# Kernel tuning notes

Measured on AMD Instinct MI355X. Metric: run time of the kernel, lower is better.

The kernel has to match this reference:

```python
import jax, jax.numpy as jnp
import numpy as np

D, N, P, K = 128, 500000, 1024, 32


def setup_inputs() -> dict:
    key = jax.random.key(0)
    k1, k2, k3, k4 = jax.random.split(key, 4)
    U_base = jax.random.normal(k1, (D, N), dtype=jnp.float32)
    U = jax.random.normal(k2, (D, P), dtype=jnp.float32)
    # ragged partition: column j of U_base belongs to group seg_ids[j]
    merge_idx = jnp.arange(N, dtype=jnp.int64)
    seg_ids = jnp.sort(jax.random.randint(k3, (N,), 0, P)).astype(jnp.int64)
    # k nearest-neighbor indices per group for the Gram gather
    G = jax.random.randint(k4, (P, K), 0, P).astype(jnp.int64)
    return {"U_base": U_base, "U": U, "merge_idx": merge_idx,
            "seg_ids": seg_ids, "G": G}


def reference(U_base, U, merge_idx, seg_ids, G):
    # Flattened ragged loop: for each column j in group g = seg_ids[j],
    # dot(U[:, g], U_base[:, merge_idx[j]]); sum over dim 0 then square.
    dots = jnp.sum(U_base[:, merge_idx] * U[:, seg_ids], axis=0)  # [N]
    loss = -0.5 * jnp.sum(dots ** 2)
    # Gram-matrix neighbor gather: (U.T @ U)[G] -> [P, K, P]
    gram = U.T @ U  # [P, P]
    loss = loss - 0.5 * jnp.mean(gram[G] ** 2)
    return loss
```

## Files before the change

kernel.cpp:

```cpp
#include <hip/hip_runtime.h>

#define DIM 128
#define NCOLS 500000
#define PP 1024
#define KK 32


__global__ void init_ws_kernel(float* __restrict__ wsf) {
    int i = blockIdx.x * blockDim.x + threadIdx.x;
    if (i < 2) wsf[i] = 0.0f;
    int* counts = (int*)(wsf + 2);
    if (i < PP) counts[i] = 0;
}

__global__ void hist_kernel(const int* __restrict__ G, int* __restrict__ counts) {
    int i = blockIdx.x * blockDim.x + threadIdx.x;
    if (i < PP * KK) atomicAdd(&counts[G[i]], 1);
}

__global__ void gram_m_kernel(const float* __restrict__ U, float* __restrict__ M) {
    int t = blockIdx.x * blockDim.x + threadIdx.x;
    int d = t >> 7, e = t & 127;
    const float4* ud = (const float4*)(U + (size_t)d * PP);
    const float4* ue = (const float4*)(U + (size_t)e * PP);
    float acc = 0.0f;
#pragma unroll 4
    for (int p = 0; p < PP / 4; ++p) {
        float4 a = ud[p], b = ue[p];
        acc += a.x * b.x + a.y * b.y + a.z * b.z + a.w * b.w;
    }
    M[t] = acc;
}

__global__ void rowsq_kernel(const float* __restrict__ U, const float* __restrict__ M,
                             const int* __restrict__ counts, float* __restrict__ acc_out) {
    __shared__ float u_s[DIM];
    __shared__ float red[DIM];
    int r = blockIdx.x;
    int d = threadIdx.x;
    u_s[d] = U[(size_t)d * PP + r];
    __syncthreads();
    float t = 0.0f;
#pragma unroll 8
    for (int e = 0; e < DIM; ++e)
        t += M[e * DIM + d] * u_s[e];
    float v = u_s[d] * t;
    red[d] = v;
    __syncthreads();
    for (int s = 64; s > 0; s >>= 1) {
        if (d < s) red[d] += red[d + s];
        __syncthreads();
    }
    if (d == 0) atomicAdd(acc_out, red[0] * (float)counts[r]);
}

__global__ void __launch_bounds__(256) dots_kernel(
    const float* __restrict__ U_base, const float* __restrict__ U,
    const int* __restrict__ merge_idx, const int* __restrict__ seg_ids,
    float* __restrict__ acc_out) {
    int t = blockIdx.x * blockDim.x + threadIdx.x;
    int j0 = t * 4;
    float a0 = 0.f, a1 = 0.f, a2 = 0.f, a3 = 0.f;
    if (j0 < NCOLS) {
        int4 m = ((const int4*)merge_idx)[t];
        int4 g = ((const int4*)seg_ids)[t];
        bool contig = (m.y == m.x + 1) & (m.z == m.x + 2) & (m.w == m.x + 3) & ((m.x & 3) == 0);
        bool sameg = (g.x == g.w);
        if (contig & sameg) {
            const float* ub = U_base + m.x;
            const float* up = U + g.x;
#pragma unroll 4
            for (int d = 0; d < DIM; ++d) {
                float4 b = *(const float4*)(ub + (size_t)d * NCOLS);
                float ug = up[(size_t)d * PP];
                a0 += b.x * ug; a1 += b.y * ug; a2 += b.z * ug; a3 += b.w * ug;
            }
        } else {
            for (int d = 0; d < DIM; ++d) {
                size_t rb = (size_t)d * NCOLS;
                size_t ru = (size_t)d * PP;
                a0 += U_base[rb + m.x] * U[ru + g.x];
                a1 += U_base[rb + m.y] * U[ru + g.y];
                a2 += U_base[rb + m.z] * U[ru + g.z];
                a3 += U_base[rb + m.w] * U[ru + g.w];
            }
        }
    }
    float local = a0 * a0 + a1 * a1 + a2 * a2 + a3 * a3;
    __shared__ float red[256];
    red[threadIdx.x] = local;
    __syncthreads();
    for (int s = 128; s > 0; s >>= 1) {
        if (threadIdx.x < s) red[threadIdx.x] += red[threadIdx.x + s];
        __syncthreads();
    }
    if (threadIdx.x == 0) atomicAdd(acc_out, red[0]);
}

__global__ void finalize_kernel(const float* __restrict__ wsf, float* __restrict__ out) {
    out[0] = -0.5f * wsf[0] - 0.5f * (wsf[1] * (1.0f / 33554432.0f));
}

extern "C" void kernel_launch(void* const* d_in, const int* in_sizes, int n_in,
                              void* d_out, int out_size, void* d_ws, size_t ws_size,
                              hipStream_t stream) {
    const float* U_base  = (const float*)d_in[0];
    const float* U       = (const float*)d_in[1];
    const int* merge_idx = (const int*)d_in[2];
    const int* seg_ids   = (const int*)d_in[3];
    const int* G         = (const int*)d_in[4];
    float* out = (float*)d_out;

    float* wsf   = (float*)d_ws;
    int* counts  = (int*)(wsf + 2);
    float* M     = wsf + 2 + PP;

    init_ws_kernel<<<4, 256, 0, stream>>>(wsf);
    hist_kernel<<<(PP * KK + 255) / 256, 256, 0, stream>>>(G, counts);
    gram_m_kernel<<<64, 256, 0, stream>>>(U, M);

    int n_threads = NCOLS / 4;
    int n_blocks = (n_threads + 255) / 256;
    dots_kernel<<<n_blocks, 256, 0, stream>>>(U_base, U, merge_idx, seg_ids, &wsf[0]);

    rowsq_kernel<<<PP, DIM, 0, stream>>>(U, M, counts, &wsf[1]);
    finalize_kernel<<<1, 1, 0, stream>>>(wsf, out);
}
```

Measured before the change: 441.4 us.

## Split dots kernel across D chunks with 2D blocks and nontemporal loads

The dots kernel now gives each block 64 column-groups by 4 D-chunks of 32 rows, so each thread reduces only a quarter of the dimension. That raises the number of loads in flight and shortens each thread's serial chain. Partial sums are combined through shared memory, squared, then reduced with a wavefront shuffle instead of a tree of syncthreads. The U_base loads use nontemporal hints to avoid polluting the cache with streamed data. In exchange it adds a shared-memory combine step and launches four times as many blocks.

```diff
diff --git a/kernel.cpp b/kernel.cpp
--- a/kernel.cpp
+++ b/kernel.cpp
@@ -4,6 +4,9 @@
 #define NCOLS 500000
 #define PP 1024
 #define KK 32
+#define DCHUNK 32
+
+typedef float floatx4 __attribute__((ext_vector_type(4)));
 
 
 __global__ void init_ws_kernel(float* __restrict__ wsf) {
@@ -58,25 +61,27 @@
     const float* __restrict__ U_base, const float* __restrict__ U,
     const int* __restrict__ merge_idx, const int* __restrict__ seg_ids,
     float* __restrict__ acc_out) {
-    int t = blockIdx.x * blockDim.x + threadIdx.x;
-    int j0 = t * 4;
+    const int x = threadIdx.x;
+    const int y = threadIdx.y;
+    const int tcol = blockIdx.x * 64 + x;
     float a0 = 0.f, a1 = 0.f, a2 = 0.f, a3 = 0.f;
-    if (j0 < NCOLS) {
-        int4 m = ((const int4*)merge_idx)[t];
-        int4 g = ((const int4*)seg_ids)[t];
+    if (tcol < NCOLS / 4) {
+        int4 m = ((const int4*)merge_idx)[tcol];
+        int4 g = ((const int4*)seg_ids)[tcol];
+        const int d0 = y * DCHUNK;
         bool contig = (m.y == m.x + 1) & (m.z == m.x + 2) & (m.w == m.x + 3) & ((m.x & 3) == 0);
         bool sameg = (g.x == g.w);
         if (contig & sameg) {
-            const float* ub = U_base + m.x;
-            const float* up = U + g.x;
-#pragma unroll 4
-            for (int d = 0; d < DIM; ++d) {
-                float4 b = *(const float4*)(ub + (size_t)d * NCOLS);
+            const float* ub = U_base + (size_t)d0 * NCOLS + m.x;
+            const float* up = U + (size_t)d0 * PP + g.x;
+#pragma unroll 8
+            for (int d = 0; d < DCHUNK; ++d) {
+                floatx4 b = __builtin_nontemporal_load((const floatx4*)(ub + (size_t)d * NCOLS));
                 float ug = up[(size_t)d * PP];
                 a0 += b.x * ug; a1 += b.y * ug; a2 += b.z * ug; a3 += b.w * ug;
             }
         } else {
-            for (int d = 0; d < DIM; ++d) {
+            for (int d = d0; d < d0 + DCHUNK; ++d) {
                 size_t rb = (size_t)d * NCOLS;
                 size_t ru = (size_t)d * PP;
                 a0 += U_base[rb + m.x] * U[ru + g.x];
@@ -86,15 +91,21 @@
             }
         }
     }
-    float local = a0 * a0 + a1 * a1 + a2 * a2 + a3 * a3;
-    __shared__ float red[256];
-    red[threadIdx.x] = local;
+    __shared__ float4 red[256];
+    red[y * 64 + x] = make_float4(a0, a1, a2, a3);
     __syncthreads();
-    for (int s = 128; s > 0; s >>= 1) {
-        if (threadIdx.x < s) red[threadIdx.x] += red[threadIdx.x + s];
-        __syncthreads();
+    if (y == 0) {
+        float s0 = 0.f, s1 = 0.f, s2 = 0.f, s3 = 0.f;
+#pragma unroll
+        for (int yy = 0; yy < 4; ++yy) {
+            float4 r = red[yy * 64 + x];
+            s0 += r.x; s1 += r.y; s2 += r.z; s3 += r.w;
+        }
+        float v = s0 * s0 + s1 * s1 + s2 * s2 + s3 * s3;
+#pragma unroll
+        for (int off = 32; off > 0; off >>= 1) v += __shfl_down(v, off, 64);
+        if (x == 0) atomicAdd(acc_out, v);
     }
-    if (threadIdx.x == 0) atomicAdd(acc_out, red[0]);
 }
 
 __global__ void finalize_kernel(const float* __restrict__ wsf, float* __restrict__ out) {
@@ -119,9 +130,10 @@
     hist_kernel<<<(PP * KK + 255) / 256, 256, 0, stream>>>(G, counts);
     gram_m_kernel<<<64, 256, 0, stream>>>(U, M);
 
-    int n_threads = NCOLS / 4;
-    int n_blocks = (n_threads + 255) / 256;
-    dots_kernel<<<n_blocks, 256, 0, stream>>>(U_base, U, merge_idx, seg_ids, &wsf[0]);
+    int n_groups = NCOLS / 4;
+    int n_blocks = (n_groups + 63) / 64;
+    dim3 blk(64, 4);
+    dots_kernel<<<n_blocks, blk, 0, stream>>>(U_base, U, merge_idx, seg_ids, &wsf[0]);
 
     rowsq_kernel<<<PP, DIM, 0, stream>>>(U, M, counts, &wsf[1]);
     finalize_kernel<<<1, 1, 0, stream>>>(wsf, out);
```

Result: faster. 418.7 us (-5.1%).
